# Performance work log

Measured on AMD Instinct MI355X. Metric: run time of the kernel, lower is better.

Reference implementation:

```python
import jax, jax.numpy as jnp
import numpy as np

NEG = -9e9  # large negative used by the original torch code for masking


def setup_inputs() -> dict:
    key = jax.random.key(0)
    k1, k2, k3, k4 = jax.random.split(key, 4)
    B, N, L, D = 64, 128, 64, 768
    return {
        "text_embeddings": jax.random.normal(k1, (B, N, D), dtype=jnp.float32),
        "image_embeddings": jax.random.normal(k2, (B, L, D), dtype=jnp.float32),
        "text_mask": jax.random.randint(k3, (B, N), 0, 2, dtype=jnp.int32),
        "image_mask": jax.random.randint(k4, (B, L), 0, 2, dtype=jnp.int32),
    }


def _grounding(text_emb, image_emb, text_mask, image_mask):
    # Vectorized version of the B x B python loop in score_grounding.
    tm = text_mask.astype(text_emb.dtype)   # [B, N]
    im = image_mask.astype(text_emb.dtype)  # [B, L]
    # pairwise mask: mask[i, j, n, l] = text_mask[i, n] * image_mask[j, l]
    mask = tm[:, None, :, None] * im[None, :, None, :]            # [B, B, N, L]
    att = jnp.einsum('ind,jld->ijnl', text_emb, image_emb) * mask  # [B, B, N, L]
    att = jnp.where(att * mask != 0, att, NEG)
    # softmax over image spans (last dim), masked
    aw_first = jax.nn.softmax(att, axis=-1) * mask
    score1 = (aw_first * att).sum(-1).mean(-1)                     # [B, B]
    # softmax over text spans (dim 2 == the N axis), masked (transpose trick in torch)
    aw_second = jax.nn.softmax(att, axis=2) * mask
    score2 = (aw_second * att).sum(-1).mean(-1)                    # [B, B]
    sent_scores = score1 + score2                                  # [B, B]
    B = text_emb.shape[0]
    idx = jnp.arange(B)
    token_scores = att[idx, idx]                                   # diagonal pairs, [B, N, L]
    return sent_scores, token_scores


def reference(text_embeddings, image_embeddings, text_mask, image_mask):
    B = text_embeddings.shape[0]
    S, token_scores = _grounding(text_embeddings, image_embeddings, text_mask, image_mask)
    # text_emb_i2s = softmax(att_weights) @ image_emb
    text_emb_i2s = jnp.einsum('bnl,bld->bnd', jax.nn.softmax(token_scores, axis=-1), image_embeddings)
    # loss = -(sum diag logsoftmax(S, dim=1) + sum diag logsoftmax(S.T, dim=1)) / n
    ls1 = jnp.diagonal(jax.nn.log_softmax(S, axis=1))
    ls2 = jnp.diagonal(jax.nn.log_softmax(S.T, axis=1))
    loss = -(jnp.sum(ls1) + jnp.sum(ls2)) / B
    return loss, text_emb_i2s
```

## Files before the change

kernel.cpp:

```cpp
#include <hip/hip_runtime.h>
#include <math.h>

#define BSZ 64
#define NN  128
#define LL  64
#define DD  768
#define NEGV (-9e9f)

#define TQ (BSZ * NN * DD / 4)
#define IQ (BSZ * LL * DD / 4)

typedef _Float16 f16x8 __attribute__((ext_vector_type(8)));
typedef __attribute__((ext_vector_type(4))) float f32x4;

__device__ __forceinline__ void gl_lds16(const void* g, void* l) {
    __builtin_amdgcn_global_load_lds(
        (const __attribute__((address_space(1))) void*)g,
        (__attribute__((address_space(3))) void*)l, 16, 0, 0);
}

__global__ __launch_bounds__(256) void k_prep(
    const float4* __restrict__ t4, const float4* __restrict__ g4,
    ushort4* __restrict__ A, ushort4* __restrict__ B)
{
    int id = blockIdx.x * 256 + threadIdx.x;
    const float4* src; ushort4* dst; int idx;
    if (id < TQ) { src = t4; dst = A; idx = id; }
    else         { src = g4; dst = B; idx = id - TQ; }
    float4 x = src[idx];
    _Float16 h0 = (_Float16)x.x, h1 = (_Float16)x.y;
    _Float16 h2 = (_Float16)x.z, h3 = (_Float16)x.w;
    ushort4 o;
    o.x = __builtin_bit_cast(unsigned short, h0);
    o.y = __builtin_bit_cast(unsigned short, h1);
    o.z = __builtin_bit_cast(unsigned short, h2);
    o.w = __builtin_bit_cast(unsigned short, h3);
    dst[idx] = o;
}

__device__ __forceinline__ void stage_chunk(
    const unsigned short* __restrict__ pa, const unsigned short* __restrict__ pb,
    int k0, char* buf, int wave, int lane)
{
    int rsub = lane >> 3;
    int k8s  = lane & 7;
#pragma unroll
    for (int c = 0; c < 4; c++) {
        int r  = c * 32 + wave * 8 + rsub;
        int k8 = k8s ^ (r & 7);
        gl_lds16(pa + (size_t)r * DD + k0 + k8 * 8, buf + c * 4096 + wave * 1024);
        gl_lds16(pb + (size_t)r * DD + k0 + k8 * 8, buf + 16384 + c * 4096 + wave * 1024);
    }
}

__global__ __launch_bounds__(256, 2) void k_scores(
    const unsigned short* __restrict__ A, const unsigned short* __restrict__ B,
    const int* __restrict__ tmask, const int* __restrict__ imask,
    float* __restrict__ S, float* __restrict__ W)
{
    union SmemU {
        char  stage[2][32768];
        float Cs[NN][129];
    };
    __shared__ SmemU u;
    __shared__ float tmi[NN];
    __shared__ float imj[NN];
    __shared__ float rowred[256];
    __shared__ float colred[NN];
    __shared__ float rowm[256], rowsm[256];
    __shared__ float colm[256], colp1[256], colp2[256];

    const int bid = blockIdx.x;
    const int grp = bid >> 4, idx = bid & 15;
    const int i  = (grp >> 3) * 4 + (idx >> 2);
    const int jj = (grp & 7) * 4 + (idx & 3);
    const int j0 = jj * 2;

    const int tid  = threadIdx.x;
    const int wave = tid >> 6;
    const int lane = tid & 63;
    const int quad = lane >> 4;
    const int l15  = lane & 15;
    const int rh   = wave & 1;
    const int ch   = wave >> 1;

    if (tid < NN) {
        tmi[tid] = tmask[i * NN + tid] ? 1.f : 0.f;
        imj[tid] = imask[j0 * LL + tid] ? 1.f : 0.f;
    }

    const unsigned short* pa = A + (size_t)i * NN * DD;
    const unsigned short* pb = B + (size_t)j0 * LL * DD;

    f32x4 acc[4][4];
    const f32x4 zf = {0.f, 0.f, 0.f, 0.f};
#pragma unroll
    for (int tr = 0; tr < 4; tr++)
#pragma unroll
        for (int tc = 0; tc < 4; tc++) acc[tr][tc] = zf;

    stage_chunk(pa, pb, 0, u.stage[0], wave, lane);
    __syncthreads();

    for (int c = 0; c < 12; c++) {
        if (c + 1 < 12)
            stage_chunk(pa, pb, (c + 1) << 6, u.stage[(c + 1) & 1], wave, lane);
        const char* Ab = u.stage[c & 1];
        const char* Bb = Ab + 16384;
#pragma unroll
        for (int s = 0; s < 2; s++) {
            int k8q = s * 4 + quad;
            int sw  = k8q ^ (l15 & 7);
            f16x8 af[4], bfr[4];
#pragma unroll
            for (int t = 0; t < 4; t++) {
                int row = rh * 64 + t * 16 + l15;
                af[t]  = *(const f16x8*)(Ab + ((row << 3) + sw) * 16);
                int col = ch * 64 + t * 16 + l15;
                bfr[t] = *(const f16x8*)(Bb + ((col << 3) + sw) * 16);
            }
#pragma unroll
            for (int tr = 0; tr < 4; tr++)
#pragma unroll
                for (int tc = 0; tc < 4; tc++)
                    acc[tr][tc] = __builtin_amdgcn_mfma_f32_16x16x32_f16(
                        af[tr], bfr[tc], acc[tr][tc], 0, 0, 0);
        }
        __syncthreads();
    }

#pragma unroll
    for (int tr = 0; tr < 4; tr++) {
        int rb = rh * 64 + tr * 16 + quad * 4;
#pragma unroll
        for (int tc = 0; tc < 4; tc++) {
            int col = ch * 64 + tc * 16 + l15;
            float im = imj[col];
#pragma unroll
            for (int rr = 0; rr < 4; rr++) {
                int row = rb + rr;
                float v = acc[tr][tc][rr];
                bool keep = (tmi[row] != 0.f) && (im != 0.f) && (v != 0.f);
                u.Cs[row][col] = keep ? v : NEGV;
            }
        }
    }
    __syncthreads();

    {
        int jh = tid >> 7, n = tid & 127;
        const float* Crow = &u.Cs[n][jh * 64];
        float m = -INFINITY;
        for (int l = 0; l < LL; l++) m = fmaxf(m, Crow[l]);
        float ssum = 0.f, ws = 0.f;
        for (int l = 0; l < LL; l++) {
            float v = Crow[l];
            float e = __expf(v - m);
            ssum += e;
            ws += imj[jh * 64 + l] * e * v;
        }
        rowm[tid] = m;
        rowsm[tid] = ssum;
        rowred[tid] = tmi[n] * (ws / ssum);
    }
    __syncthreads();

    {
        int c  = tid & 127;
        int n0 = (tid >> 7) * 64;
        float m = -INFINITY;
        for (int n = n0; n < n0 + 64; n++) m = fmaxf(m, u.Cs[n][c]);
        colm[tid] = m;
        __syncthreads();
        m = fmaxf(colm[tid], colm[tid ^ 128]);
        float ssum = 0.f, ws = 0.f;
        for (int n = n0; n < n0 + 64; n++) {
            float v = u.Cs[n][c];
            float e = __expf(v - m);
            ssum += e;
            ws += tmi[n] * e * v;
        }
        colp1[tid] = ssum;
        colp2[tid] = ws;
    }
    __syncthreads();
    if (tid < NN) {
        float ssum = colp1[tid] + colp1[tid + 128];
        float ws   = colp2[tid] + colp2[tid + 128];
        colred[tid] = imj[tid] * (ws / ssum);
    }

    if (jj == (i >> 1) && tid < NN) {
        int jh = i & 1;
        int n = tid;
        float m   = rowm[jh * 128 + n];
        float inv = 1.f / rowsm[jh * 128 + n];
        const float* Crow = &u.Cs[n][jh * 64];
        float* Wb = W + (size_t)i * LL * NN;
        for (int l = 0; l < LL; l++)
            Wb[(size_t)l * NN + n] = __expf(Crow[l] - m) * inv;
    }
    __syncthreads();

    if (tid < NN) {
        int jh = tid >> 6, t = tid & 63;
        float p = rowred[jh * 128 + t] + rowred[jh * 128 + 64 + t] + colred[jh * 64 + t];
#pragma unroll
        for (int off = 32; off; off >>= 1) p += __shfl_down(p, off);
        if (t == 0) S[i * BSZ + j0 + jh] = p / (float)NN;
    }
}

__global__ __launch_bounds__(256) void k_i2s(
    const float* __restrict__ W, const float* __restrict__ img,
    const float* __restrict__ S, float* __restrict__ out)
{
    __shared__ float Ws[LL][16];
    const int b  = blockIdx.x;
    const int ng = blockIdx.z * 16;
    const int d  = blockIdx.y * 256 + threadIdx.x;
    const float* Wb = W + (size_t)b * LL * NN;

    {
        int t4 = threadIdx.x * 4;
        int l = t4 >> 4, noff = t4 & 15;
        float4 w = *(const float4*)(Wb + (size_t)l * NN + ng + noff);
        Ws[l][noff + 0] = w.x; Ws[l][noff + 1] = w.y;
        Ws[l][noff + 2] = w.z; Ws[l][noff + 3] = w.w;
    }
    __syncthreads();

    const float* ib = img + (size_t)b * LL * DD;
    float* ob = out + 1 + (size_t)b * NN * DD + (size_t)ng * DD;

    float acc[16];
#pragma unroll
    for (int q = 0; q < 16; q++) acc[q] = 0.f;
    for (int l = 0; l < LL; l++) {
        float g = ib[(size_t)l * DD + d];
#pragma unroll
        for (int q = 0; q < 16; q++)
            acc[q] = fmaf(Ws[l][q], g, acc[q]);
    }
#pragma unroll
    for (int q = 0; q < 16; q++)
        ob[(size_t)q * DD + d] = acc[q];

    if (blockIdx.x == 0 && blockIdx.y == 0 && blockIdx.z == 0 && threadIdx.x < 64) {
        const int t = threadIdx.x;
        float diag = S[t * BSZ + t];
        float m1 = -INFINITY, m2 = -INFINITY;
        for (int jj = 0; jj < BSZ; jj++) {
            m1 = fmaxf(m1, S[t * BSZ + jj]);
            m2 = fmaxf(m2, S[jj * BSZ + t]);
        }
        float s1 = 0.f, s2 = 0.f;
        for (int jj = 0; jj < BSZ; jj++) {
            s1 += __expf(S[t * BSZ + jj] - m1);
            s2 += __expf(S[jj * BSZ + t] - m2);
        }
        float p = 2.f * diag - (m1 + logf(s1)) - (m2 + logf(s2));
#pragma unroll
        for (int off = 32; off; off >>= 1) p += __shfl_down(p, off);
        if (t == 0) out[0] = -p / (float)BSZ;
    }
}

extern "C" void kernel_launch(void* const* d_in, const int* in_sizes, int n_in,
                              void* d_out, int out_size, void* d_ws, size_t ws_size,
                              hipStream_t stream)
{
    (void)in_sizes; (void)n_in; (void)out_size; (void)ws_size;
    const float* text = (const float*)d_in[0];
    const float* img  = (const float*)d_in[1];
    const int*   tm   = (const int*)d_in[2];
    const int*   im   = (const int*)d_in[3];
    float* out = (float*)d_out;

    char* ws = (char*)d_ws;
    unsigned short* A = (unsigned short*)(ws);
    unsigned short* B = (unsigned short*)(ws + 12582912);
    float* S = (float*)(ws + 18874368);
    float* W = (float*)(ws + 18890752);

    k_prep<<<(TQ + IQ) / 256, 256, 0, stream>>>(
        (const float4*)text, (const float4*)img, (ushort4*)A, (ushort4*)B);

    k_scores<<<BSZ * (BSZ / 2), 256, 0, stream>>>(A, B, tm, im, S, W);

    dim3 g2(BSZ, 3, 8);
    k_i2s<<<g2, 256, 0, stream>>>(W, img, S, out);
}
```

Baseline: 184.5 us.

## Retile score GEMM to 256x256 blocks with 32x32 MFMA and in-register softmax

The scores kernel now computes 256x256 output tiles (two text batches by four image batches) with 512-thread blocks and 32x32x16 MFMA instructions, instead of 128x128 tiles per block with 16x16 MFMAs. Masking and both row and column softmax reductions run directly on accumulator registers using cross-lane shuffles, so the fp32 score tile is no longer written to shared memory. The larger tile reuses each A and B chunk across more output and cuts the grid from 2048 to 512 blocks. In exchange it uses 128KB of LDS per block, which may limit occupancy to one block per CU, and adds heavier register pressure and shuffle-based reductions.

```diff
diff --git a/kernel.cpp b/kernel.cpp
--- a/kernel.cpp
+++ b/kernel.cpp
@@ -11,7 +11,7 @@
 #define IQ (BSZ * LL * DD / 4)
 
 typedef _Float16 f16x8 __attribute__((ext_vector_type(8)));
-typedef __attribute__((ext_vector_type(4))) float f32x4;
+typedef __attribute__((ext_vector_type(16))) float f32x16;
 
 __device__ __forceinline__ void gl_lds16(const void* g, void* l) {
     __builtin_amdgcn_global_load_lds(
@@ -42,172 +42,182 @@
     const unsigned short* __restrict__ pa, const unsigned short* __restrict__ pb,
     int k0, char* buf, int wave, int lane)
 {
-    int rsub = lane >> 3;
-    int k8s  = lane & 7;
-#pragma unroll
-    for (int c = 0; c < 4; c++) {
-        int r  = c * 32 + wave * 8 + rsub;
-        int k8 = k8s ^ (r & 7);
-        gl_lds16(pa + (size_t)r * DD + k0 + k8 * 8, buf + c * 4096 + wave * 1024);
-        gl_lds16(pb + (size_t)r * DD + k0 + k8 * 8, buf + 16384 + c * 4096 + wave * 1024);
-    }
-}
-
-__global__ __launch_bounds__(256, 2) void k_scores(
+#pragma unroll
+    for (int cc = 0; cc < 4; ++cc) {
+        int s  = cc * 512 + wave * 64 + lane;
+        int k8 = s >> 8, r = s & 255;
+        gl_lds16(pa + (size_t)r * DD + k0 + k8 * 8, buf + cc * 8192 + wave * 1024);
+        gl_lds16(pb + (size_t)r * DD + k0 + k8 * 8, buf + 32768 + cc * 8192 + wave * 1024);
+    }
+}
+
+__global__ __launch_bounds__(512, 2) void k_scores(
     const unsigned short* __restrict__ A, const unsigned short* __restrict__ B,
     const int* __restrict__ tmask, const int* __restrict__ imask,
     float* __restrict__ S, float* __restrict__ W)
 {
-    union SmemU {
-        char  stage[2][32768];
-        float Cs[NN][129];
-    };
-    __shared__ SmemU u;
-    __shared__ float tmi[NN];
-    __shared__ float imj[NN];
-    __shared__ float rowred[256];
-    __shared__ float colred[NN];
-    __shared__ float rowm[256], rowsm[256];
-    __shared__ float colm[256], colp1[256], colp2[256];
+    __shared__ __align__(16) char smem[131072];
+    char* buf0 = smem;
+    char* buf1 = smem + 65536;
 
     const int bid = blockIdx.x;
     const int grp = bid >> 4, idx = bid & 15;
-    const int i  = (grp >> 3) * 4 + (idx >> 2);
-    const int jj = (grp & 7) * 4 + (idx & 3);
-    const int j0 = jj * 2;
+    const int tm = (grp >> 2) * 4 + (idx >> 2);
+    const int tn = (grp & 3) * 4 + (idx & 3);
 
     const int tid  = threadIdx.x;
     const int wave = tid >> 6;
     const int lane = tid & 63;
-    const int quad = lane >> 4;
-    const int l15  = lane & 15;
-    const int rh   = wave & 1;
-    const int ch   = wave >> 1;
-
-    if (tid < NN) {
-        tmi[tid] = tmask[i * NN + tid] ? 1.f : 0.f;
-        imj[tid] = imask[j0 * LL + tid] ? 1.f : 0.f;
-    }
-
-    const unsigned short* pa = A + (size_t)i * NN * DD;
-    const unsigned short* pb = B + (size_t)j0 * LL * DD;
-
-    f32x4 acc[4][4];
-    const f32x4 zf = {0.f, 0.f, 0.f, 0.f};
-#pragma unroll
-    for (int tr = 0; tr < 4; tr++)
-#pragma unroll
-        for (int tc = 0; tc < 4; tc++) acc[tr][tc] = zf;
-
-    stage_chunk(pa, pb, 0, u.stage[0], wave, lane);
+    const int l31  = lane & 31;
+    const int hi   = lane >> 5;
+    const int wm   = wave >> 2;
+    const int wn   = wave & 3;
+
+    const unsigned short* pa = A + (size_t)tm * 256 * DD;
+    const unsigned short* pb = B + (size_t)tn * 256 * DD;
+
+    const f32x16 zf16 = {0.f,0.f,0.f,0.f,0.f,0.f,0.f,0.f,
+                         0.f,0.f,0.f,0.f,0.f,0.f,0.f,0.f};
+    f32x16 acc[4][2];
+#pragma unroll
+    for (int mt = 0; mt < 4; ++mt)
+#pragma unroll
+        for (int nt = 0; nt < 2; ++nt) acc[mt][nt] = zf16;
+
+    stage_chunk(pa, pb, 0, buf0, wave, lane);
     __syncthreads();
 
-    for (int c = 0; c < 12; c++) {
+    for (int c = 0; c < 12; ++c) {
+        char* cur = (c & 1) ? buf1 : buf0;
         if (c + 1 < 12)
-            stage_chunk(pa, pb, (c + 1) << 6, u.stage[(c + 1) & 1], wave, lane);
-        const char* Ab = u.stage[c & 1];
-        const char* Bb = Ab + 16384;
-#pragma unroll
-        for (int s = 0; s < 2; s++) {
-            int k8q = s * 4 + quad;
-            int sw  = k8q ^ (l15 & 7);
-            f16x8 af[4], bfr[4];
-#pragma unroll
-            for (int t = 0; t < 4; t++) {
-                int row = rh * 64 + t * 16 + l15;
-                af[t]  = *(const f16x8*)(Ab + ((row << 3) + sw) * 16);
-                int col = ch * 64 + t * 16 + l15;
-                bfr[t] = *(const f16x8*)(Bb + ((col << 3) + sw) * 16);
+            stage_chunk(pa, pb, (c + 1) << 6, (c & 1) ? buf0 : buf1, wave, lane);
+#pragma unroll
+        for (int s16 = 0; s16 < 4; ++s16) {
+            const int k8 = s16 * 2 + hi;
+            f16x8 af[4], bf[2];
+#pragma unroll
+            for (int mt = 0; mt < 4; ++mt)
+                af[mt] = *(const f16x8*)(cur + ((k8 << 8) + wm * 128 + mt * 32 + l31) * 16);
+#pragma unroll
+            for (int nt = 0; nt < 2; ++nt)
+                bf[nt] = *(const f16x8*)(cur + 32768 + ((k8 << 8) + wn * 64 + nt * 32 + l31) * 16);
+#pragma unroll
+            for (int mt = 0; mt < 4; ++mt)
+#pragma unroll
+                for (int nt = 0; nt < 2; ++nt)
+                    acc[mt][nt] = __builtin_amdgcn_mfma_f32_32x32x16_f16(
+                        af[mt], bf[nt], acc[mt][nt], 0, 0, 0);
+        }
+        __syncthreads();
+    }
+
+    float* msk   = (float*)smem;
+    float* rowmL = (float*)smem + 512;
+    float* rowsL = (float*)smem + 768;
+    if (tid < 256) msk[tid] = tmask[tm * 256 + tid] ? 1.f : 0.f;
+    else           msk[tid] = imask[tn * 256 + (tid - 256)] ? 1.f : 0.f;
+    __syncthreads();
+
+    const float imv0 = msk[256 + wn * 64 + l31];
+    const float imv1 = msk[256 + wn * 64 + 32 + l31];
+
+#pragma unroll
+    for (int mt = 0; mt < 4; ++mt) {
+#pragma unroll
+        for (int q = 0; q < 16; ++q) {
+            int rl = (q & 3) + 8 * (q >> 2) + 4 * hi;
+            float tmv = msk[wm * 128 + mt * 32 + rl];
+            float v0 = acc[mt][0][q];
+            float v1 = acc[mt][1][q];
+            acc[mt][0][q] = (tmv != 0.f && imv0 != 0.f && v0 != 0.f) ? v0 : NEGV;
+            acc[mt][1][q] = (tmv != 0.f && imv1 != 0.f && v1 != 0.f) ? v1 : NEGV;
+        }
+    }
+
+    const bool diagw = (tm * 2 + wm) == (tn * 4 + wn);
+
+    float srow = 0.f;
+#pragma unroll
+    for (int mt = 0; mt < 4; ++mt) {
+#pragma unroll
+        for (int q = 0; q < 16; ++q) {
+            float v0 = acc[mt][0][q], v1 = acc[mt][1][q];
+            float m = fmaxf(v0, v1);
+#pragma unroll
+            for (int d = 1; d <= 16; d <<= 1) m = fmaxf(m, __shfl_xor(m, d));
+            float e0 = __expf(v0 - m), e1 = __expf(v1 - m);
+            float ss = e0 + e1;
+            float ws = imv0 * e0 * v0 + imv1 * e1 * v1;
+#pragma unroll
+            for (int d = 1; d <= 16; d <<= 1) {
+                ss += __shfl_xor(ss, d);
+                ws += __shfl_xor(ws, d);
             }
-#pragma unroll
-            for (int tr = 0; tr < 4; tr++)
-#pragma unroll
-                for (int tc = 0; tc < 4; tc++)
-                    acc[tr][tc] = __builtin_amdgcn_mfma_f32_16x16x32_f16(
-                        af[tr], bfr[tc], acc[tr][tc], 0, 0, 0);
-        }
-        __syncthreads();
-    }
-
-#pragma unroll
-    for (int tr = 0; tr < 4; tr++) {
-        int rb = rh * 64 + tr * 16 + quad * 4;
-#pragma unroll
-        for (int tc = 0; tc < 4; tc++) {
-            int col = ch * 64 + tc * 16 + l15;
-            float im = imj[col];
-#pragma unroll
-            for (int rr = 0; rr < 4; rr++) {
-                int row = rb + rr;
-                float v = acc[tr][tc][rr];
-                bool keep = (tmi[row] != 0.f) && (im != 0.f) && (v != 0.f);
-                u.Cs[row][col] = keep ? v : NEGV;
+            int rl = (q & 3) + 8 * (q >> 2) + 4 * hi;
+            float tmv = msk[wm * 128 + mt * 32 + rl];
+            srow += tmv * (ws / ss);
+            if (diagw && l31 == 0) {
+                rowmL[wm * 128 + mt * 32 + rl] = m;
+                rowsL[wm * 128 + mt * 32 + rl] = ss;
             }
         }
     }
+    srow += __shfl_xor(srow, 32);
+
+    float scol = 0.f;
+#pragma unroll
+    for (int nt = 0; nt < 2; ++nt) {
+        float m = -INFINITY;
+#pragma unroll
+        for (int mt = 0; mt < 4; ++mt)
+#pragma unroll
+            for (int q = 0; q < 16; ++q) m = fmaxf(m, acc[mt][nt][q]);
+        m = fmaxf(m, __shfl_xor(m, 32));
+        float ss = 0.f, ws = 0.f;
+#pragma unroll
+        for (int mt = 0; mt < 4; ++mt)
+#pragma unroll
+            for (int q = 0; q < 16; ++q) {
+                int rl = (q & 3) + 8 * (q >> 2) + 4 * hi;
+                float tmv = msk[wm * 128 + mt * 32 + rl];
+                float v = acc[mt][nt][q];
+                float e = __expf(v - m);
+                ss += e;
+                ws += tmv * e * v;
+            }
+        ss += __shfl_xor(ss, 32);
+        ws += __shfl_xor(ws, 32);
+        float imv = nt ? imv1 : imv0;
+        scol += imv * (ws / ss);
+    }
+#pragma unroll
+    for (int d = 1; d <= 32; d <<= 1) scol += __shfl_xor(scol, d);
+    scol *= 0.5f;
+
+    if (lane == 0)
+        S[(tm * 2 + wm) * BSZ + (tn * 4 + wn)] = (srow + scol) / (float)NN;
+
     __syncthreads();
 
-    {
-        int jh = tid >> 7, n = tid & 127;
-        const float* Crow = &u.Cs[n][jh * 64];
-        float m = -INFINITY;
-        for (int l = 0; l < LL; l++) m = fmaxf(m, Crow[l]);
-        float ssum = 0.f, ws = 0.f;
-        for (int l = 0; l < LL; l++) {
-            float v = Crow[l];
-            float e = __expf(v - m);
-            ssum += e;
-            ws += imj[jh * 64 + l] * e * v;
-        }
-        rowm[tid] = m;
-        rowsm[tid] = ssum;
-        rowred[tid] = tmi[n] * (ws / ssum);
-    }
-    __syncthreads();
-
-    {
-        int c  = tid & 127;
-        int n0 = (tid >> 7) * 64;
-        float m = -INFINITY;
-        for (int n = n0; n < n0 + 64; n++) m = fmaxf(m, u.Cs[n][c]);
-        colm[tid] = m;
-        __syncthreads();
-        m = fmaxf(colm[tid], colm[tid ^ 128]);
-        float ssum = 0.f, ws = 0.f;
-        for (int n = n0; n < n0 + 64; n++) {
-            float v = u.Cs[n][c];
-            float e = __expf(v - m);
-            ssum += e;
-            ws += tmi[n] * e * v;
-        }
-        colp1[tid] = ssum;
-        colp2[tid] = ws;
-    }
-    __syncthreads();
-    if (tid < NN) {
-        float ssum = colp1[tid] + colp1[tid + 128];
-        float ws   = colp2[tid] + colp2[tid + 128];
-        colred[tid] = imj[tid] * (ws / ssum);
-    }
-
-    if (jj == (i >> 1) && tid < NN) {
-        int jh = i & 1;
-        int n = tid;
-        float m   = rowm[jh * 128 + n];
-        float inv = 1.f / rowsm[jh * 128 + n];
-        const float* Crow = &u.Cs[n][jh * 64];
-        float* Wb = W + (size_t)i * LL * NN;
-        for (int l = 0; l < LL; l++)
-            Wb[(size_t)l * NN + n] = __expf(Crow[l] - m) * inv;
-    }
-    __syncthreads();
-
-    if (tid < NN) {
-        int jh = tid >> 6, t = tid & 63;
-        float p = rowred[jh * 128 + t] + rowred[jh * 128 + 64 + t] + colred[jh * 64 + t];
-#pragma unroll
-        for (int off = 32; off; off >>= 1) p += __shfl_down(p, off);
-        if (t == 0) S[i * BSZ + j0 + jh] = p / (float)NN;
+    if (diagw) {
+        float* Wb = W + (size_t)(tm * 2 + wm) * LL * NN;
+#pragma unroll
+        for (int nt = 0; nt < 2; ++nt) {
+            int col = wn * 64 + nt * 32 + l31;
+#pragma unroll
+            for (int mt = 0; mt < 4; ++mt) {
+#pragma unroll
+                for (int qq = 0; qq < 4; ++qq) {
+                    int n0 = mt * 32 + 8 * qq + 4 * hi;
+                    float4 w;
+                    w.x = __expf(acc[mt][nt][qq * 4 + 0] - rowmL[wm * 128 + n0 + 0]) / rowsL[wm * 128 + n0 + 0];
+                    w.y = __expf(acc[mt][nt][qq * 4 + 1] - rowmL[wm * 128 + n0 + 1]) / rowsL[wm * 128 + n0 + 1];
+                    w.z = __expf(acc[mt][nt][qq * 4 + 2] - rowmL[wm * 128 + n0 + 2]) / rowsL[wm * 128 + n0 + 2];
+                    w.w = __expf(acc[mt][nt][qq * 4 + 3] - rowmL[wm * 128 + n0 + 3]) / rowsL[wm * 128 + n0 + 3];
+                    *(float4*)(Wb + ((size_t)col & 63) * NN + n0) = w;
+                }
+            }
+        }
     }
 }
 
@@ -286,7 +296,7 @@
     k_prep<<<(TQ + IQ) / 256, 256, 0, stream>>>(
         (const float4*)text, (const float4*)img, (ushort4*)A, (ushort4*)B);
 
-    k_scores<<<BSZ * (BSZ / 2), 256, 0, stream>>>(A, B, tm, im, S, W);
+    k_scores<<<512, 512, 0, stream>>>(A, B, tm, im, S, W);
 
     dim3 g2(BSZ, 3, 8);
     k_i2s<<<g2, 256, 0, stream>>>(W, img, S, out);
```

Result: slower. 341.5 us (+85.1%).
